# Performance work log

Measured on AMD Instinct MI355X. Metric: run time of the kernel, lower is better.

## Reference

```python
import jax, jax.numpy as jnp
import numpy as np

KERNEL = 5
OUT_CAPS = 8
OUT_ATOMS = 32
ROUTINGS = 3


def _squash(x):
    # squash nonlinearity: (|v|^2 / (1+|v|^2)) * v/|v|, over last (atom) axis
    norm = jnp.linalg.norm(x, axis=-1, keepdims=True)
    norm_sq = norm * norm
    return (x / norm) * (norm_sq / (1.0 + norm_sq))


def setup_inputs() -> dict:
    key = jax.random.key(0)
    k1, k2, k3 = jax.random.split(key, 3)
    B, H, Wd, inC, inA = 16, 32, 32, 8, 16
    inputs = jax.random.normal(k1, (B, H, Wd, inC, inA), dtype=jnp.float32)
    # He-normal-ish conv kernel [k, k, inA, outC*outA]
    fan_in = KERNEL * KERNEL * inA
    W = jax.random.normal(k2, (KERNEL, KERNEL, inA, OUT_CAPS * OUT_ATOMS), dtype=jnp.float32) * np.sqrt(2.0 / fan_in)
    b = jnp.full((1, 1, OUT_CAPS, OUT_ATOMS), 0.1, dtype=jnp.float32)
    return {"inputs": inputs, "W": W, "b": b}


def reference(inputs, W, b):
    B, H, Wd, inC, inA = inputs.shape
    # transpose to [inC, B, H, W, inA] and fold capsules into batch for shared conv
    x = jnp.transpose(inputs, (3, 0, 1, 2, 4)).reshape(inC * B, H, Wd, inA)
    conv = jax.lax.conv_general_dilated(
        x, W, window_strides=(1, 1), padding="SAME",
        dimension_numbers=("NHWC", "HWIO", "NHWC"))
    Hp, Wp = conv.shape[1], conv.shape[2]
    # faithful to original TF reshape (row-major) of [inC*B,...] -> [B, inC, ...]
    votes = conv.reshape(B, inC, Hp, Wp, OUT_CAPS, OUT_ATOMS)
    biases = jnp.broadcast_to(b, (Hp, Wp, OUT_CAPS, OUT_ATOMS))

    logits = jnp.zeros((B, inC, Hp, Wp, OUT_CAPS), dtype=votes.dtype)
    act = None
    for _ in range(ROUTINGS):
        route = jax.nn.softmax(logits, axis=-1)  # over output capsules
        # weighted sum of votes over input capsules: [B, Hp, Wp, outC, outA]
        preact = jnp.einsum("bihwc,bihwca->bhwca", route, votes) + biases
        act = _squash(preact)
        # agreement: dot(votes, activation) over atoms -> logit update
        logits = logits + jnp.sum(votes * act[:, None], axis=-1)
    return act
```

## Files before the change

### kernel.cpp

```cpp
#include <hip/hip_runtime.h>


typedef __attribute__((ext_vector_type(2))) _Float16 f16x2;
typedef __attribute__((ext_vector_type(8))) _Float16 f16x8;
typedef __attribute__((ext_vector_type(16))) float f32x16;

union f16x8u { f16x8 v; f16x2 d[4]; unsigned short s[8]; unsigned int u32[4]; unsigned long long u[2]; };
union f16x2u { f16x2 v; unsigned int u; unsigned short s[2]; };

__device__ __forceinline__ unsigned short f2h(float x) {
  union { _Float16 h; unsigned short u; } v;
  v.h = (_Float16)x;
  return v.u;
}

template<int CTRL>
__device__ __forceinline__ float dpp_mov(float x) {
  return __builtin_bit_cast(float, __builtin_amdgcn_update_dpp(
      0, __builtin_bit_cast(int, x), CTRL, 0xF, 0xF, true));
}
__device__ __forceinline__ float sum8_dpp(float x) {
  x += dpp_mov<0xB1>(x);
  x += dpp_mov<0x4E>(x);
  x += dpp_mov<0x141>(x);
  return x;
}

__global__ __launch_bounds__(256) void wprep_kernel(
    const float* __restrict__ W, unsigned short* __restrict__ wsh) {
  int t = blockIdx.x * 256 + threadIdx.x;
  int khkw = t >> 12;
  int rem  = t & 4095;
  int ch = rem >> 4, ia = rem & 15;
  wsh[t] = f2h(W[khkw * 4096 + ia * 256 + ch]);
}

__global__ __launch_bounds__(256, 2) void capsconv_mfma_kernel(
    const float* __restrict__ inp,
    const unsigned short* __restrict__ wsh,
    const float* __restrict__ bias,
    float* __restrict__ out)
{
  __shared__ char smem[36864];
  const _Float16* wshh = (const _Float16*)wsh;

  const int tid  = threadIdx.x;
  const int wid  = tid >> 6;
  const int lane = tid & 63;
  const int sub  = lane >> 5;
  const int ln31 = lane & 31;

  const int bid = blockIdx.x;
  const int wq = bid & 3;
  const int h  = (bid >> 2) & 31;
  const int bb = bid >> 7;
  const int i_src  = bb >> 1;
  const int b_base = (bb & 1) * 8;

  for (int e = tid; e < 1920; e += 256) {
    int kh = e / 384; int r1 = e - kh * 384;
    int ii = r1 / 48; int r2 = r1 - ii * 48;
    int wl = r2 >> 2; int iaq = r2 & 3;
    int hh = h + kh - 2;
    int wsrc = wq * 8 + wl - 2;
    float4 v = make_float4(0.f, 0.f, 0.f, 0.f);
    if ((unsigned)hh < 32u && (unsigned)wsrc < 32u)
      v = *(const float4*)(inp +
          ((((size_t)(b_base + ii) * 32 + hh) * 32 + wsrc) * 8 + i_src) * 16 + iaq * 4);
    union { _Float16 hx[4]; unsigned long long u; } pkk;
    pkk.hx[0] = (_Float16)v.x; pkk.hx[1] = (_Float16)v.y;
    pkk.hx[2] = (_Float16)v.z; pkk.hx[3] = (_Float16)v.w;
    *(unsigned long long*)(smem + kh * 3200 + ii * 400 + wl * 32 + iaq * 8) = pkk.u;
  }
  __syncthreads();

  f32x16 acc[2][2];
  #pragma unroll
  for (int mt = 0; mt < 2; ++mt)
    #pragma unroll
    for (int nt = 0; nt < 2; ++nt)
      #pragma unroll
      for (int e = 0; e < 16; ++e) acc[mt][nt][e] = 0.f;

  const char* aBase = smem + (ln31 & 7) * 400 + (ln31 >> 3) * 32 + sub * 16;
  const _Float16* bBase = wshh + (wid * 64 + ln31) * 16 + sub * 8;

  #pragma unroll
  for (int kh = 0; kh < 5; ++kh) {
    #pragma unroll
    for (int kw = 0; kw < 5; ++kw) {
      f16x8 af0 = *(const f16x8*)(aBase + kh * 3200 + kw * 32);
      f16x8 af1 = *(const f16x8*)(aBase + kh * 3200 + (kw + 4) * 32);
      f16x8 bf0 = *(const f16x8*)(bBase + (size_t)(kh * 5 + kw) * 4096);
      f16x8 bf1 = *(const f16x8*)(bBase + (size_t)(kh * 5 + kw) * 4096 + 512);
      acc[0][0] = __builtin_amdgcn_mfma_f32_32x32x16_f16(af0, bf0, acc[0][0], 0, 0, 0);
      acc[0][1] = __builtin_amdgcn_mfma_f32_32x32x16_f16(af0, bf1, acc[0][1], 0, 0, 0);
      acc[1][0] = __builtin_amdgcn_mfma_f32_32x32x16_f16(af1, bf0, acc[1][0], 0, 0, 0);
      acc[1][1] = __builtin_amdgcn_mfma_f32_32x32x16_f16(af1, bf1, acc[1][1], 0, 0, 0);
    }
  }

  __syncthreads();
  #pragma unroll
  for (int mt = 0; mt < 2; ++mt)
    #pragma unroll
    for (int nt = 0; nt < 2; ++nt) {
      int ch = wid * 64 + nt * 32 + ln31;
      char* base = smem + (ch >> 2) * 72 + (ch & 3) * 16 + sub * 8;
      #pragma unroll
      for (int q = 0; q < 4; ++q) {
        f16x2u lo, hi;
        lo.v = f16x2{(_Float16)acc[mt][nt][q * 4 + 0], (_Float16)acc[mt][nt][q * 4 + 1]};
        hi.v = f16x2{(_Float16)acc[mt][nt][q * 4 + 2], (_Float16)acc[mt][nt][q * 4 + 3]};
        unsigned long long u = (unsigned long long)lo.u |
                               ((unsigned long long)hi.u << 32);
        *(unsigned long long*)(base + (mt * 4 + q) * 4608) = u;
      }
    }
  __syncthreads();

  const int k = lane & 7;
  float vv[2][4][8];
  #pragma unroll
  for (int p = 0; p < 2; ++p)
    #pragma unroll
    for (int j = 0; j < 4; ++j) {
      f16x8u t8;
      t8.v = *(const f16x8*)(smem + (wid * 2 + p) * 4608 + lane * 72 + j * 16);
      #pragma unroll
      for (int ii = 0; ii < 8; ++ii) vv[p][j][ii] = (float)t8.v[ii];
    }
  const float4 bv4 = *(const float4*)(bias + lane * 4);
  const float bvj[4] = {bv4.x, bv4.y, bv4.z, bv4.w};

  float logit_k[2] = {0.f, 0.f};
  float pre[2][4], scale[2] = {0.f, 0.f};

  #pragma unroll
  for (int rt = 0; rt < 3; ++rt) {
    #pragma unroll
    for (int p = 0; p < 2; ++p) {
      float r[8];
      if (rt == 0) {
        #pragma unroll
        for (int i = 0; i < 8; ++i) r[i] = 0.125f;
      } else {
        float mx = logit_k[p];
        mx = fmaxf(mx, dpp_mov<0x128>(mx));
        mx = fmaxf(mx, __shfl_xor(mx, 16, 64));
        mx = fmaxf(mx, __shfl_xor(mx, 32, 64));
        float e = __expf(logit_k[p] - mx);
        float den = e;
        den += dpp_mov<0x128>(den);
        den += __shfl_xor(den, 16, 64);
        den += __shfl_xor(den, 32, 64);
        float route_k = e / den;
        int cbase = lane & 56;
        #pragma unroll
        for (int i = 0; i < 8; ++i) r[i] = __shfl(route_k, cbase | i, 64);
      }
      #pragma unroll
      for (int j = 0; j < 4; ++j) {
        float pp = bvj[j];
        #pragma unroll
        for (int ii = 0; ii < 8; ++ii) pp = fmaf(r[ii], vv[p][j][ii], pp);
        pre[p][j] = pp;
      }
      float nsq = pre[p][0] * pre[p][0] + pre[p][1] * pre[p][1] +
                  pre[p][2] * pre[p][2] + pre[p][3] * pre[p][3];
      nsq = sum8_dpp(nsq);
      scale[p] = sqrtf(nsq) / (1.f + nsq);
      if (rt < 2) {
        float dot8[8];
        #pragma unroll
        for (int ii = 0; ii < 8; ++ii) {
          float d = vv[p][0][ii] * pre[p][0];
          d = fmaf(vv[p][1][ii], pre[p][1], d);
          d = fmaf(vv[p][2][ii], pre[p][2], d);
          d = fmaf(vv[p][3][ii], pre[p][3], d);
          dot8[ii] = sum8_dpp(d);
        }
        bool b0 = (k & 1), b1 = (k & 2), b2 = (k & 4);
        float e0 = b0 ? dot8[1] : dot8[0];
        float e1 = b0 ? dot8[3] : dot8[2];
        float e2 = b0 ? dot8[5] : dot8[4];
        float e3 = b0 ? dot8[7] : dot8[6];
        float f0 = b1 ? e1 : e0;
        float f1 = b1 ? e3 : e2;
        logit_k[p] = fmaf(scale[p], b2 ? f1 : f0, logit_k[p]);
      }
    }
  }
  const size_t base8 = (size_t)((bb * 32 + h) * 32 + wq * 8);
  #pragma unroll
  for (int p = 0; p < 2; ++p) {
    float4 o = make_float4(pre[p][0] * scale[p], pre[p][1] * scale[p],
                           pre[p][2] * scale[p], pre[p][3] * scale[p]);
    *(float4*)(out + (base8 + wid * 2 + p) * 256 + lane * 4) = o;
  }
}

extern "C" void kernel_launch(void* const* d_in, const int* in_sizes, int n_in,
                              void* d_out, int out_size, void* d_ws, size_t ws_size,
                              hipStream_t stream) {
  (void)in_sizes; (void)n_in; (void)ws_size; (void)out_size;
  const float* inp  = (const float*)d_in[0];
  const float* W    = (const float*)d_in[1];
  const float* bv   = (const float*)d_in[2];
  float* out        = (float*)d_out;
  unsigned short* wsh = (unsigned short*)d_ws;

  hipLaunchKernelGGL(wprep_kernel, dim3(400), dim3(256), 0, stream, W, wsh);
  hipLaunchKernelGGL(capsconv_mfma_kernel, dim3(2048), dim3(256), 0, stream,
                     inp, wsh, bv, out);
}
```

Before: 49.53 us.

## Halve epilogue LDS staging by processing M-tiles in two passes, raise occupancy

```diff
diff --git a/kernel.cpp b/kernel.cpp
--- a/kernel.cpp
+++ b/kernel.cpp
@@ -35,13 +35,13 @@
   wsh[t] = f2h(W[khkw * 4096 + ia * 256 + ch]);
 }
 
-__global__ __launch_bounds__(256, 2) void capsconv_mfma_kernel(
+__global__ __launch_bounds__(256, 4) void capsconv_mfma_kernel(
     const float* __restrict__ inp,
     const unsigned short* __restrict__ wsh,
     const float* __restrict__ bias,
     float* __restrict__ out)
 {
-  __shared__ char smem[36864];
+  __shared__ char smem[18432];
   const _Float16* wshh = (const _Float16*)wsh;
 
   const int tid  = threadIdx.x;
@@ -100,36 +100,39 @@
     }
   }
 
-  __syncthreads();
-  #pragma unroll
-  for (int mt = 0; mt < 2; ++mt)
-    #pragma unroll
-    for (int nt = 0; nt < 2; ++nt) {
-      int ch = wid * 64 + nt * 32 + ln31;
-      char* base = smem + (ch >> 2) * 72 + (ch & 3) * 16 + sub * 8;
+  float vv[2][4][8];
+  {
+    const int ch0 = wid * 64 + ln31;
+    char* base0 = smem + (ch0 >> 2) * 72 + (ch0 & 3) * 16 + sub * 8;
+    const int ch1 = ch0 + 32;
+    char* base1 = smem + (ch1 >> 2) * 72 + (ch1 & 3) * 16 + sub * 8;
+    #pragma unroll
+    for (int mt = 0; mt < 2; ++mt) {
+      __syncthreads();
       #pragma unroll
       for (int q = 0; q < 4; ++q) {
-        f16x2u lo, hi;
-        lo.v = f16x2{(_Float16)acc[mt][nt][q * 4 + 0], (_Float16)acc[mt][nt][q * 4 + 1]};
-        hi.v = f16x2{(_Float16)acc[mt][nt][q * 4 + 2], (_Float16)acc[mt][nt][q * 4 + 3]};
-        unsigned long long u = (unsigned long long)lo.u |
-                               ((unsigned long long)hi.u << 32);
-        *(unsigned long long*)(base + (mt * 4 + q) * 4608) = u;
+        f16x2u lo0, hi0, lo1, hi1;
+        lo0.v = f16x2{(_Float16)acc[mt][0][q * 4 + 0], (_Float16)acc[mt][0][q * 4 + 1]};
+        hi0.v = f16x2{(_Float16)acc[mt][0][q * 4 + 2], (_Float16)acc[mt][0][q * 4 + 3]};
+        lo1.v = f16x2{(_Float16)acc[mt][1][q * 4 + 0], (_Float16)acc[mt][1][q * 4 + 1]};
+        hi1.v = f16x2{(_Float16)acc[mt][1][q * 4 + 2], (_Float16)acc[mt][1][q * 4 + 3]};
+        *(unsigned long long*)(base0 + q * 4608) =
+            (unsigned long long)lo0.u | ((unsigned long long)hi0.u << 32);
+        *(unsigned long long*)(base1 + q * 4608) =
+            (unsigned long long)lo1.u | ((unsigned long long)hi1.u << 32);
+      }
+      __syncthreads();
+      #pragma unroll
+      for (int j = 0; j < 4; ++j) {
+        f16x8u t8;
+        t8.v = *(const f16x8*)(smem + wid * 4608 + lane * 72 + j * 16);
+        #pragma unroll
+        for (int ii = 0; ii < 8; ++ii) vv[mt][j][ii] = (float)t8.v[ii];
       }
     }
-  __syncthreads();
+  }
 
   const int k = lane & 7;
-  float vv[2][4][8];
-  #pragma unroll
-  for (int p = 0; p < 2; ++p)
-    #pragma unroll
-    for (int j = 0; j < 4; ++j) {
-      f16x8u t8;
-      t8.v = *(const f16x8*)(smem + (wid * 2 + p) * 4608 + lane * 72 + j * 16);
-      #pragma unroll
-      for (int ii = 0; ii < 8; ++ii) vv[p][j][ii] = (float)t8.v[ii];
-    }
   const float4 bv4 = *(const float4*)(bias + lane * 4);
   const float bvj[4] = {bv4.x, bv4.y, bv4.z, bv4.w};
 
@@ -196,7 +199,7 @@
   for (int p = 0; p < 2; ++p) {
     float4 o = make_float4(pre[p][0] * scale[p], pre[p][1] * scale[p],
                            pre[p][2] * scale[p], pre[p][3] * scale[p]);
-    *(float4*)(out + (base8 + wid * 2 + p) * 256 + lane * 4) = o;
+    *(float4*)(out + (base8 + wid + 4 * p) * 256 + lane * 4) = o;
   }
 }
 
```

Result: no change. 49.72 us (+0.4%).
